# Optimization experiments

Measured on AMD Instinct MI355X. Metric: run time of the kernel, lower is better.

The kernel has to match this reference:

```python
import jax, jax.numpy as jnp
import numpy as np

B, C, H, W = 32, 32, 64, 64   # batch, in_channel, image height/width
HC = 1                        # hashtable channel groups (in_channel % HC == 0)
KS = 9                        # kernel_size: top-k neighbors per pixel
K = 64                        # kernel_number_per_pixel (output channels)
P = H * W                     # pixel_number


def setup_inputs() -> dict:
    key = jax.random.key(0)
    k1, k2, k3 = jax.random.split(key, 3)
    x = jax.random.normal(k1, (B, C, H, W), dtype=jnp.float32)
    # Per-pixel affinity scores -> top-KS neighbor indices (mimics
    # _build_full_hash: argsort descending, take first kernel_size).
    scores = jax.random.normal(k2, (HC, H, W, P), dtype=jnp.float32)
    idx = jnp.argsort(-scores, axis=-1)[..., :KS].astype(jnp.int32)  # (HC, NH, NW, KS)
    bound = float(np.sqrt(1.0 / (C * KS)))
    weights = jax.random.uniform(k3, (K, C * KS), minval=-bound, maxval=bound,
                                 dtype=jnp.float32)
    return {"x": x, "weights": weights, "idx": idx}


def reference(x, weights, idx):
    Bx, Cx, Hx, Wx = x.shape
    HCx, NH, NW, ks = idx.shape
    Px = Hx * Wx
    # full_hash[b, c, i, j, k] = idx[c % HC, i, j, k] + c*P + b*C*P,
    # so x.take(full_hash) == gather of x[b, c] at idx[c % HC].
    idx_full = jnp.tile(idx, (Cx // HCx, 1, 1, 1)).reshape(Cx, NH * NW * ks)
    g = jnp.take_along_axis(x.reshape(Bx, Cx, Px), idx_full[None], axis=2)  # (B, C, NH*NW*ks)
    # permute(1,4,0,2,3).reshape(C*ks, B*NH*NW)
    g = g.reshape(Bx, Cx, NH, NW, ks).transpose(1, 4, 0, 2, 3).reshape(Cx * ks, Bx * NH * NW)
    out = (weights @ g).reshape(-1, Bx, NH, NW)  # (K, B, NH, NW)
    return jnp.transpose(out, (1, 0, 2, 3))       # (B, K, NH, NW)
```

## Files before the change

### kernel.cpp

```cpp
#include <hip/hip_runtime.h>
#include <hip/hip_bf16.h>

#define BB 32
#define CC 32
#define PP 4096
#define KS 9
#define KK 64
#define CK 288

typedef __attribute__((ext_vector_type(8))) short short8;
typedef __attribute__((ext_vector_type(4))) float float4v;

__device__ inline unsigned short f2bf(float f) {
    __hip_bfloat16 h = __float2bfloat16(f);
    return __builtin_bit_cast(unsigned short, h);
}

__global__ __launch_bounds__(256)
void prep_xt_kernel(const float* __restrict__ x, unsigned short* __restrict__ xt) {
    const int t = threadIdx.x;
    const int b = blockIdx.x >> 4;
    const int p = ((blockIdx.x & 15) << 8) + t;
    const float* xb = x + (size_t)b * CC * PP + p;
    unsigned int buf[16];
#pragma unroll
    for (int c2 = 0; c2 < 16; ++c2) {
        float lo = xb[(size_t)(2 * c2) * PP];
        float hi = xb[(size_t)(2 * c2 + 1) * PP];
        buf[c2] = (unsigned int)f2bf(lo) | ((unsigned int)f2bf(hi) << 16);
    }
    uint4* dst = (uint4*)(xt + ((size_t)b * PP + p) * CC);
    const uint4* s = (const uint4*)buf;
#pragma unroll
    for (int j = 0; j < 4; ++j) dst[j] = s[j];
}

__global__ void prep_wb_kernel(const float* __restrict__ w,
                               unsigned short* __restrict__ wb, int n) {
    int i = blockIdx.x * blockDim.x + threadIdx.x;
    if (i >= n) return;
    int j  = i & 7;
    int l  = (i >> 3) & 63;
    int nt = (i >> 9) & 3;
    int kc = i >> 11;
    int c  = ((l >> 4) << 3) + j;
    int nn = (nt << 4) + (l & 15);
    wb[i] = f2bf(w[nn * CK + c * KS + kc]);
}

__global__ __launch_bounds__(256)
void abc_mfma_kernel(const unsigned short* __restrict__ xt,
                     const unsigned short* __restrict__ wb,
                     const int* __restrict__ idx,
                     float* __restrict__ out) {
    __shared__ char smem[74752];
    unsigned short* As = (unsigned short*)smem;
    unsigned short* Bs = (unsigned short*)(smem + 37888);
    float* Cs = (float*)smem;

    const int t  = threadIdx.x;
    const int b  = blockIdx.x >> 6;
    const int p0 = (blockIdx.x & 63) << 6;

    {
        const uint4* src = (const uint4*)wb;
        uint4* dst = (uint4*)Bs;
#pragma unroll
        for (int j = 0; j < 9; ++j) dst[j * 256 + t] = src[j * 256 + t];
    }
    {
#pragma unroll
        for (int j = 0; j < 9; ++j) {
            int id  = j * 256 + t;
            int g   = id >> 2, sub = id & 3;
            int pl  = g / 9;
            int k   = g - pl * 9;
            int q   = idx[(p0 + pl) * KS + k];
            const uint4* src = (const uint4*)(xt + ((size_t)b * PP + q) * CC + (sub << 3));
            *(uint4*)(&As[pl * 296 + k * 32 + (sub << 3)]) = *src;
        }
    }
    __syncthreads();

    const int l    = t & 63;
    const int w    = t >> 6;
    const int lo16 = l & 15;
    const int quad = l >> 4;

    float4v acc[4] = {{0,0,0,0},{0,0,0,0},{0,0,0,0},{0,0,0,0}};

#pragma unroll
    for (int kc = 0; kc < 9; ++kc) {
        short8 a = *(const short8*)(&As[(w * 16 + lo16) * 296 + kc * 32 + quad * 8]);
#pragma unroll
        for (int nt = 0; nt < 4; ++nt) {
            short8 bf = *(const short8*)(&Bs[(((kc * 4 + nt) * 64) + l) * 8]);
            acc[nt] = __builtin_amdgcn_mfma_f32_16x16x32_bf16(a, bf, acc[nt], 0, 0, 0);
        }
    }
    __syncthreads();

#pragma unroll
    for (int nt = 0; nt < 4; ++nt)
#pragma unroll
        for (int r = 0; r < 4; ++r)
            Cs[(nt * 16 + lo16) * 68 + (w * 16 + quad * 4 + r)] = acc[nt][r];
    __syncthreads();

    float* ob = out + (size_t)b * KK * PP + p0;
#pragma unroll
    for (int j = 0; j < 4; ++j) {
        int fid = j * 256 + t;
        int ko  = fid >> 4, pm = fid & 15;
        float4v v = *(const float4v*)(&Cs[ko * 68 + pm * 4]);
        *(float4v*)(ob + (size_t)ko * PP + pm * 4) = v;
    }
}

__global__ __launch_bounds__(256)
void abc_valu_kernel(const float* __restrict__ x, const float* __restrict__ w,
                     const int* __restrict__ idx, float* __restrict__ out) {
    __shared__ float xrow[PP];
    const int t = threadIdx.x;
    const int b = blockIdx.x >> 4;
    const int p = ((blockIdx.x & 15) << 8) + t;
    int q[KS];
#pragma unroll
    for (int k = 0; k < KS; ++k) q[k] = idx[p * KS + k];
    float acc[KK];
#pragma unroll
    for (int i = 0; i < KK; ++i) acc[i] = 0.0f;
    const float* xb = x + (size_t)b * CC * PP;
#pragma unroll 1
    for (int c = 0; c < CC; ++c) {
        const float4* src = (const float4*)(xb + (size_t)c * PP);
        float4* dst = (float4*)xrow;
#pragma unroll
        for (int j = 0; j < 4; ++j) dst[j * 256 + t] = src[j * 256 + t];
        __syncthreads();
        float xv[KS];
#pragma unroll
        for (int k = 0; k < KS; ++k) xv[k] = xrow[q[k]];
#pragma unroll
        for (int k = 0; k < KS; ++k) {
            const int col = c * KS + k;
#pragma unroll
            for (int ko = 0; ko < KK; ++ko)
                acc[ko] += xv[k] * w[ko * CK + col];
        }
        __syncthreads();
    }
    float* ob = out + (size_t)b * KK * PP + p;
#pragma unroll
    for (int ko = 0; ko < KK; ++ko)
        ob[(size_t)ko * PP] = acc[ko];
}

extern "C" void kernel_launch(void* const* d_in, const int* in_sizes, int n_in,
                              void* d_out, int out_size, void* d_ws, size_t ws_size,
                              hipStream_t stream) {
    const float* x  = (const float*)d_in[0];
    const float* w  = (const float*)d_in[1];
    const int* idx  = (const int*)d_in[2];
    float* out      = (float*)d_out;

    const size_t xt_bytes = (size_t)BB * PP * CC * 2;
    const size_t wb_off   = xt_bytes;
    const size_t need     = xt_bytes + (size_t)KK * CK * 2;

    if (ws_size >= need) {
        unsigned short* xt = (unsigned short*)d_ws;
        unsigned short* wbp = (unsigned short*)((char*)d_ws + wb_off);
        prep_xt_kernel<<<BB * (PP / 256), 256, 0, stream>>>(x, xt);
        prep_wb_kernel<<<(KK * CK + 255) / 256, 256, 0, stream>>>(w, wbp, KK * CK);
        abc_mfma_kernel<<<BB * (PP / 64), 256, 0, stream>>>(xt, wbp, idx, out);
    } else {
        abc_valu_kernel<<<BB * (PP / 256), 256, 0, stream>>>(x, w, idx, out);
    }
}
```

Measured before the change: 98.40 us.

## Merge prep kernels and gather MFMA operands directly from global memory

Folds the two preprocessing kernels into one launch that splits work by block index. The MFMA kernel drops shared memory entirely: it swaps operand roles so weights form the A fragment and gathered pixel rows form the B fragment, loaded straight from global memory (weights from L2, which all blocks share). Each wave handles 32 pixels with 8 accumulators, and results are written to global memory directly instead of being transposed through shared memory. This removes the LDS staging, the barriers, and one launch, but trades them for more scattered global loads and narrower output stores.

```diff
diff --git a/kernel.cpp b/kernel.cpp
--- a/kernel.cpp
+++ b/kernel.cpp
@@ -17,103 +17,87 @@
 }
 
 __global__ __launch_bounds__(256)
-void prep_xt_kernel(const float* __restrict__ x, unsigned short* __restrict__ xt) {
+void prep_kernel(const float* __restrict__ x, const float* __restrict__ w,
+                 unsigned short* __restrict__ xt, unsigned short* __restrict__ wa) {
     const int t = threadIdx.x;
-    const int b = blockIdx.x >> 4;
-    const int p = ((blockIdx.x & 15) << 8) + t;
-    const float* xb = x + (size_t)b * CC * PP + p;
-    unsigned int buf[16];
+    const int blk = blockIdx.x;
+    if (blk < 512) {
+        const int b = blk >> 4;
+        const int p = ((blk & 15) << 8) + t;
+        const float* xb = x + (size_t)b * CC * PP + p;
+        unsigned int buf[16];
 #pragma unroll
-    for (int c2 = 0; c2 < 16; ++c2) {
-        float lo = xb[(size_t)(2 * c2) * PP];
-        float hi = xb[(size_t)(2 * c2 + 1) * PP];
-        buf[c2] = (unsigned int)f2bf(lo) | ((unsigned int)f2bf(hi) << 16);
+        for (int c2 = 0; c2 < 16; ++c2) {
+            float lo = xb[(size_t)(2 * c2) * PP];
+            float hi = xb[(size_t)(2 * c2 + 1) * PP];
+            buf[c2] = (unsigned int)f2bf(lo) | ((unsigned int)f2bf(hi) << 16);
+        }
+        uint4* dst = (uint4*)(xt + ((size_t)b * PP + p) * CC);
+        const uint4* s = (const uint4*)buf;
+#pragma unroll
+        for (int j = 0; j < 4; ++j) dst[j] = s[j];
+    } else {
+        int i = (blk - 512) * 256 + t;
+        if (i < KK * CK) {
+            int j  = i & 7;
+            int l  = (i >> 3) & 63;
+            int mt = (i >> 9) & 3;
+            int kc = i >> 11;
+            int c  = ((l >> 4) << 3) + j;
+            int ko = (mt << 4) + (l & 15);
+            wa[i] = f2bf(w[ko * CK + c * KS + kc]);
+        }
     }
-    uint4* dst = (uint4*)(xt + ((size_t)b * PP + p) * CC);
-    const uint4* s = (const uint4*)buf;
-#pragma unroll
-    for (int j = 0; j < 4; ++j) dst[j] = s[j];
-}
-
-__global__ void prep_wb_kernel(const float* __restrict__ w,
-                               unsigned short* __restrict__ wb, int n) {
-    int i = blockIdx.x * blockDim.x + threadIdx.x;
-    if (i >= n) return;
-    int j  = i & 7;
-    int l  = (i >> 3) & 63;
-    int nt = (i >> 9) & 3;
-    int kc = i >> 11;
-    int c  = ((l >> 4) << 3) + j;
-    int nn = (nt << 4) + (l & 15);
-    wb[i] = f2bf(w[nn * CK + c * KS + kc]);
 }
 
 __global__ __launch_bounds__(256)
-void abc_mfma_kernel(const unsigned short* __restrict__ xt,
-                     const unsigned short* __restrict__ wb,
-                     const int* __restrict__ idx,
-                     float* __restrict__ out) {
-    __shared__ char smem[74752];
-    unsigned short* As = (unsigned short*)smem;
-    unsigned short* Bs = (unsigned short*)(smem + 37888);
-    float* Cs = (float*)smem;
-
-    const int t  = threadIdx.x;
-    const int b  = blockIdx.x >> 6;
-    const int p0 = (blockIdx.x & 63) << 6;
-
-    {
-        const uint4* src = (const uint4*)wb;
-        uint4* dst = (uint4*)Bs;
-#pragma unroll
-        for (int j = 0; j < 9; ++j) dst[j * 256 + t] = src[j * 256 + t];
-    }
-    {
-#pragma unroll
-        for (int j = 0; j < 9; ++j) {
-            int id  = j * 256 + t;
-            int g   = id >> 2, sub = id & 3;
-            int pl  = g / 9;
-            int k   = g - pl * 9;
-            int q   = idx[(p0 + pl) * KS + k];
-            const uint4* src = (const uint4*)(xt + ((size_t)b * PP + q) * CC + (sub << 3));
-            *(uint4*)(&As[pl * 296 + k * 32 + (sub << 3)]) = *src;
-        }
-    }
-    __syncthreads();
-
+void abc_mfma2_kernel(const unsigned short* __restrict__ xt,
+                      const unsigned short* __restrict__ wa,
+                      const int* __restrict__ idx,
+                      float* __restrict__ out) {
+    const int t    = threadIdx.x;
     const int l    = t & 63;
     const int w    = t >> 6;
+    const int b    = blockIdx.x >> 5;
+    const int p0   = ((blockIdx.x & 31) << 7) + (w << 5);
     const int lo16 = l & 15;
     const int quad = l >> 4;
 
-    float4v acc[4] = {{0,0,0,0},{0,0,0,0},{0,0,0,0},{0,0,0,0}};
+    const unsigned short* xtb = xt + (size_t)b * PP * CC;
 
+    float4v acc[8];
 #pragma unroll
+    for (int i = 0; i < 8; ++i) acc[i] = (float4v){0.f, 0.f, 0.f, 0.f};
+
+#pragma unroll 3
     for (int kc = 0; kc < 9; ++kc) {
-        short8 a = *(const short8*)(&As[(w * 16 + lo16) * 296 + kc * 32 + quad * 8]);
+        short8 bf[2];
 #pragma unroll
-        for (int nt = 0; nt < 4; ++nt) {
-            short8 bf = *(const short8*)(&Bs[(((kc * 4 + nt) * 64) + l) * 8]);
-            acc[nt] = __builtin_amdgcn_mfma_f32_16x16x32_bf16(a, bf, acc[nt], 0, 0, 0);
+        for (int nt = 0; nt < 2; ++nt) {
+            const int pl = p0 + nt * 16 + lo16;
+            const int q  = idx[pl * KS + kc];
+            bf[nt] = *(const short8*)(xtb + (size_t)q * CC + (quad << 3));
+        }
+        const short8* wf = (const short8*)(wa) + (kc * 4) * 64 + l;
+#pragma unroll
+        for (int mt = 0; mt < 4; ++mt) {
+            short8 a = wf[mt * 64];
+#pragma unroll
+            for (int nt = 0; nt < 2; ++nt)
+                acc[mt * 2 + nt] =
+                    __builtin_amdgcn_mfma_f32_16x16x32_bf16(a, bf[nt], acc[mt * 2 + nt], 0, 0, 0);
         }
     }
-    __syncthreads();
 
+    float* ob = out + (size_t)b * KK * PP + p0 + lo16;
 #pragma unroll
-    for (int nt = 0; nt < 4; ++nt)
+    for (int mt = 0; mt < 4; ++mt) {
+        float* om = ob + (size_t)(mt * 16 + quad * 4) * PP;
 #pragma unroll
         for (int r = 0; r < 4; ++r)
-            Cs[(nt * 16 + lo16) * 68 + (w * 16 + quad * 4 + r)] = acc[nt][r];
-    __syncthreads();
-
-    float* ob = out + (size_t)b * KK * PP + p0;
 #pragma unroll
-    for (int j = 0; j < 4; ++j) {
-        int fid = j * 256 + t;
-        int ko  = fid >> 4, pm = fid & 15;
-        float4v v = *(const float4v*)(&Cs[ko * 68 + pm * 4]);
-        *(float4v*)(ob + (size_t)ko * PP + pm * 4) = v;
+            for (int nt = 0; nt < 2; ++nt)
+                om[(size_t)r * PP + nt * 16] = acc[mt * 2 + nt][r];
     }
 }
 
@@ -165,15 +149,14 @@
     float* out      = (float*)d_out;
 
     const size_t xt_bytes = (size_t)BB * PP * CC * 2;
-    const size_t wb_off   = xt_bytes;
     const size_t need     = xt_bytes + (size_t)KK * CK * 2;
 
     if (ws_size >= need) {
         unsigned short* xt = (unsigned short*)d_ws;
-        unsigned short* wbp = (unsigned short*)((char*)d_ws + wb_off);
-        prep_xt_kernel<<<BB * (PP / 256), 256, 0, stream>>>(x, xt);
-        prep_wb_kernel<<<(KK * CK + 255) / 256, 256, 0, stream>>>(w, wbp, KK * CK);
-        abc_mfma_kernel<<<BB * (PP / 64), 256, 0, stream>>>(xt, wbp, idx, out);
+        unsigned short* wa = (unsigned short*)((char*)d_ws + xt_bytes);
+        const int wb_blocks = (KK * CK + 255) / 256;
+        prep_kernel<<<512 + wb_blocks, 256, 0, stream>>>(x, w, xt, wa);
+        abc_mfma2_kernel<<<BB * (PP / 128), 256, 0, stream>>>(xt, wa, idx, out);
     } else {
         abc_valu_kernel<<<BB * (PP / 256), 256, 0, stream>>>(x, w, idx, out);
     }
```

After: 96.97 us. No clear change (-1.5%).
